# Performance work log

Measured on AMD Instinct MI355X. Metric: run time of the kernel, lower is better.

The kernel has to match this reference:

```python
import jax, jax.numpy as jnp
import numpy as np

N_NODES = 100000
N_EDGES = 1600000
NODE_F = 64
EDGE_F = 16
OUT_F = 64


def setup_inputs() -> dict:
    key = jax.random.key(0)
    k1, k2, k3, k4, k5 = jax.random.split(key, 5)
    feat = jax.random.normal(k1, (N_NODES, NODE_F), dtype=jnp.float32)
    edge_feats = jax.random.normal(k2, (N_EDGES, EDGE_F), dtype=jnp.float32)
    src = jax.random.randint(k3, (N_EDGES,), 0, N_NODES, dtype=jnp.int64)
    dst = jax.random.randint(k4, (N_EDGES,), 0, N_NODES, dtype=jnp.int64)
    # xavier-normal-ish weight, zero bias (matches reset_parameters)
    fan_in, fan_out = NODE_F + EDGE_F, OUT_F
    std = (2.0 / (fan_in + fan_out)) ** 0.5
    weight = jax.random.normal(k5, (fan_in, fan_out), dtype=jnp.float32) * std
    bias = jnp.zeros((OUT_F,), dtype=jnp.float32)
    return {"feat": feat, "edge_feats": edge_feats, "src": src, "dst": dst,
            "weight": weight, "bias": bias}


def reference(feat, edge_feats, src, dst, weight, bias):
    N = feat.shape[0]
    # in-degree based symmetric-ish norm: pow(clamp(in_deg,1), -0.5)
    deg = jax.ops.segment_sum(jnp.ones(dst.shape, dtype=feat.dtype), dst,
                              num_segments=N)
    norm = jnp.clip(deg, 1.0) ** -0.5  # [N]
    norm = norm[:, None]
    # sum over incoming edges of concat([edge_feats, h_src]).
    # sum of concat == concat of sums, so aggregate each part separately
    # (avoids materializing the per-edge concat).
    sum_e = jax.ops.segment_sum(edge_feats, dst, num_segments=N)  # [N, E_F]
    sum_h = jax.ops.segment_sum(feat[src], dst, num_segments=N)   # [N, NODE_F]
    sum_f = jnp.concatenate([sum_e, sum_h], axis=-1)              # [N, E_F+NODE_F]
    out = (sum_f * norm) @ weight
    out = out * norm + bias
    return jax.nn.selu(out)
```

## Files before the change

kernel.cpp:

```cpp
#include <hip/hip_runtime.h>
#include <math.h>

#define N_NODES 100000
#define N_EDGES 1600000
#define OUT_F   64
#define NCHUNK  98

#define EQ4      (N_EDGES / 4)
#define CNT_BLK  ((EQ4 + 255) / 256)
#define GEMM_BLK 512
#define K_E      18

typedef __attribute__((ext_vector_type(8))) short bf16x8;
typedef __attribute__((ext_vector_type(4))) float f32x4;

__device__ __forceinline__ unsigned short f2bf_rne(float f) {
    unsigned u = __float_as_uint(f);
    return (unsigned short)((u + 0x7fffu + ((u >> 16) & 1u)) >> 16);
}
__device__ __forceinline__ float bf2f(unsigned short h) {
    return __uint_as_float((unsigned)h << 16);
}

__global__ __launch_bounds__(256) void count_gemm(
    const int* __restrict__ dst, unsigned* __restrict__ bsum,
    const float* __restrict__ feat, const float* __restrict__ weight,
    unsigned short* __restrict__ G)
{
    __shared__ unsigned lbin[NCHUNK];
    int tid = threadIdx.x;

    if (blockIdx.x < CNT_BLK) {
        if (tid < NCHUNK) lbin[tid] = 0u;
        __syncthreads();
        int q = blockIdx.x * 256 + tid;
        if (q < EQ4) {
            int4 d = ((const int4*)dst)[q];
            atomicAdd(&lbin[d.x >> 10], 1u);
            atomicAdd(&lbin[d.y >> 10], 1u);
            atomicAdd(&lbin[d.z >> 10], 1u);
            atomicAdd(&lbin[d.w >> 10], 1u);
        }
        __syncthreads();
        if (tid < NCHUNK) {
            unsigned v = lbin[tid];
            if (v) atomicAdd(&bsum[tid], v);
        }
        return;
    }

    int gb = (int)blockIdx.x - CNT_BLK;
    int wv = tid >> 6, ln = tid & 63;
    int li = ln & 15, lk = ln >> 4;

    bf16x8 Whi[4][2], Wlo[4][2];
    #pragma unroll
    for (int it = 0; it < 4; ++it)
        #pragma unroll
        for (int kb = 0; kb < 2; ++kb)
            #pragma unroll
            for (int j = 0; j < 8; ++j) {
                float w = weight[(16 + kb * 32 + lk * 8 + j) * 64 + it * 16 + li];
                unsigned short h = f2bf_rne(w);
                Whi[it][kb][j] = (short)h;
                Wlo[it][kb][j] = (short)f2bf_rne(w - bf2f(h));
            }

    const int tiles = N_NODES / 16;
    for (int tile = gb * 4 + wv; tile < tiles; tile += GEMM_BLK * 4) {
        int n = tile * 16 + li;
        const float* fr = feat + (size_t)n * 64 + lk * 8;

        bf16x8 Bhi[2], Blo[2];
        #pragma unroll
        for (int kb = 0; kb < 2; ++kb) {
            float4 v0 = *(const float4*)(fr + kb * 32);
            float4 v1 = *(const float4*)(fr + kb * 32 + 4);
            float vv[8] = {v0.x, v0.y, v0.z, v0.w, v1.x, v1.y, v1.z, v1.w};
            #pragma unroll
            for (int j = 0; j < 8; ++j) {
                unsigned short h = f2bf_rne(vv[j]);
                Bhi[kb][j] = (short)h;
                Blo[kb][j] = (short)f2bf_rne(vv[j] - bf2f(h));
            }
        }

        f32x4 acc[4] = {{0.f,0.f,0.f,0.f},{0.f,0.f,0.f,0.f},
                        {0.f,0.f,0.f,0.f},{0.f,0.f,0.f,0.f}};
        #pragma unroll
        for (int kb = 0; kb < 2; ++kb)
            #pragma unroll
            for (int it = 0; it < 4; ++it) {
                acc[it] = __builtin_amdgcn_mfma_f32_16x16x32_bf16(Whi[it][kb], Bhi[kb], acc[it], 0, 0, 0);
                acc[it] = __builtin_amdgcn_mfma_f32_16x16x32_bf16(Wlo[it][kb], Bhi[kb], acc[it], 0, 0, 0);
                acc[it] = __builtin_amdgcn_mfma_f32_16x16x32_bf16(Whi[it][kb], Blo[kb], acc[it], 0, 0, 0);
            }

        #pragma unroll
        for (int it = 0; it < 4; ++it) {
            ushort4 o;
            o.x = f2bf_rne(acc[it][0]);
            o.y = f2bf_rne(acc[it][1]);
            o.z = f2bf_rne(acc[it][2]);
            o.w = f2bf_rne(acc[it][3]);
            *(ushort4*)(G + (size_t)n * 64 + it * 16 + lk * 4) = o;
        }
    }
}

__global__ __launch_bounds__(256) void bucket_scatter(
    const int* __restrict__ src, const int* __restrict__ dst,
    const unsigned* __restrict__ bsum, unsigned* __restrict__ cursor,
    unsigned long long* __restrict__ csr_pack)
{
    __shared__ unsigned ob[128], bb[128];
    __shared__ unsigned cnt[NCHUNK];
    __shared__ unsigned gb[NCHUNK];
    int tid = threadIdx.x;

    if (tid < 128) {
        unsigned v = (tid < NCHUNK) ? bsum[tid] : 0u;
        ob[tid] = v; bb[tid] = v;
    }
    if (tid < NCHUNK) cnt[tid] = 0u;
    __syncthreads();
    #pragma unroll
    for (int o = 1; o < 128; o <<= 1) {
        unsigned u = (tid < 128 && tid >= o) ? bb[tid - o] : 0u;
        __syncthreads();
        if (tid < 128) bb[tid] += u;
        __syncthreads();
    }

    int q = blockIdx.x * 256 + tid;
    bool act = q < EQ4;
    int4 d = {0,0,0,0}, s = {0,0,0,0};
    unsigned r0 = 0, r1 = 0, r2 = 0, r3 = 0;
    if (act) {
        d = ((const int4*)dst)[q];
        s = ((const int4*)src)[q];
        r0 = atomicAdd(&cnt[d.x >> 10], 1u);
        r1 = atomicAdd(&cnt[d.y >> 10], 1u);
        r2 = atomicAdd(&cnt[d.z >> 10], 1u);
        r3 = atomicAdd(&cnt[d.w >> 10], 1u);
    }
    __syncthreads();
    if (tid < NCHUNK) {
        unsigned c = cnt[tid];
        unsigned res = c ? atomicAdd(&cursor[tid], c) : 0u;
        gb[tid] = res + bb[tid] - ob[tid];
    }
    __syncthreads();
    if (act) {
        unsigned e = (unsigned)q * 4u;
        csr_pack[gb[d.x >> 10] + r0] =
            (unsigned long long)((unsigned)s.x | (((unsigned)d.x & 1023u) << 20))
            | ((unsigned long long)(e + 0u) << 32);
        csr_pack[gb[d.y >> 10] + r1] =
            (unsigned long long)((unsigned)s.y | (((unsigned)d.y & 1023u) << 20))
            | ((unsigned long long)(e + 1u) << 32);
        csr_pack[gb[d.z >> 10] + r2] =
            (unsigned long long)((unsigned)s.z | (((unsigned)d.z & 1023u) << 20))
            | ((unsigned long long)(e + 2u) << 32);
        csr_pack[gb[d.w >> 10] + r3] =
            (unsigned long long)((unsigned)s.w | (((unsigned)d.w & 1023u) << 20))
            | ((unsigned long long)(e + 3u) << 32);
    }
}

__global__ __launch_bounds__(1024) void chunk_build(
    const unsigned* __restrict__ bsum, unsigned* __restrict__ off,
    unsigned long long* __restrict__ csr_pack)
{
    __shared__ unsigned ob[128], bb[128];
    __shared__ unsigned cnt[1024];
    __shared__ unsigned ws[16];
    int t = threadIdx.x, c = blockIdx.x;

    if (t < 128) {
        unsigned v = (t < NCHUNK) ? bsum[t] : 0u;
        ob[t] = v; bb[t] = v;
    }
    cnt[t] = 0u;
    __syncthreads();
    #pragma unroll
    for (int o = 1; o < 128; o <<= 1) {
        unsigned u = (t < 128 && t >= o) ? bb[t - o] : 0u;
        __syncthreads();
        if (t < 128) bb[t] += u;
        __syncthreads();
    }
    unsigned base = bb[c] - ob[c];
    unsigned ne   = ob[c];
    __syncthreads();

    unsigned long long ev[K_E];
    unsigned rk[K_E];
    #pragma unroll
    for (int k = 0; k < K_E; ++k) {
        unsigned i = (unsigned)t + (unsigned)k * 1024u;
        if (i < ne) {
            ev[k] = csr_pack[base + i];
            rk[k] = atomicAdd(&cnt[(unsigned)(ev[k] >> 20) & 1023u], 1u);
        }
    }
    __syncthreads();

    unsigned v = cnt[t];
    unsigned x = v;
    #pragma unroll
    for (int o = 1; o < 64; o <<= 1) {
        unsigned u = __shfl_up(x, o);
        if ((t & 63) >= o) x += u;
    }
    if ((t & 63) == 63) ws[t >> 6] = x;
    __syncthreads();
    if (t < 16) {
        unsigned y = ws[t];
        #pragma unroll
        for (int o = 1; o < 16; o <<= 1) {
            unsigned u = __shfl_up(y, o);
            if (t >= o) y += u;
        }
        ws[t] = y;
    }
    __syncthreads();
    unsigned excl = ((t >> 6) ? ws[(t >> 6) - 1] : 0u) + x - v;

    int gnode = c * 1024 + t;
    if (gnode < N_NODES) off[gnode] = base + excl;
    if (c == NCHUNK - 1 && t == 0) off[N_NODES] = N_EDGES;

    __syncthreads();
    cnt[t] = base + excl;
    __syncthreads();

    #pragma unroll
    for (int k = 0; k < K_E; ++k) {
        unsigned i = (unsigned)t + (unsigned)k * 1024u;
        if (i < ne) {
            unsigned dl = (unsigned)(ev[k] >> 20) & 1023u;
            csr_pack[cnt[dl] + rk[k]] = ev[k] & 0xFFFFFFFF000FFFFFull;
        }
    }
}

__global__ __launch_bounds__(256) void gather_out(
    const unsigned short* __restrict__ G,
    const float* __restrict__ edge_feats,
    const unsigned long long* __restrict__ csr_pack,
    const unsigned* __restrict__ off,
    const float* __restrict__ weight,
    const float* __restrict__ bias,
    float* __restrict__ out)
{
    int tid = threadIdx.x;
    int wv = tid >> 6, ln = tid & 63;

    float We[16];
    #pragma unroll
    for (int k = 0; k < 16; ++k) We[k] = weight[k * 64 + ln];
    float b = bias[ln];

    const float SC = 1.0507009873554805f;
    const float AL = 1.6732632423543772f;

    int n = blockIdx.x * 4 + wv;
    if (n >= N_NODES) return;

    unsigned start = off[n], end = off[n + 1];
    float norm2 = __builtin_amdgcn_rcpf(fmaxf((float)(end - start), 1.0f));

    const int gq = ln >> 4;
    const int eq = ln >> 2;

    float gh4[4] = {0.f, 0.f, 0.f, 0.f};
    float ae4[4] = {0.f, 0.f, 0.f, 0.f};

    const ushort4* __restrict__ Gv = (const ushort4*)G;

    for (unsigned base = start; base < end; base += 64u) {
        unsigned m = min(64u, end - base);
        unsigned lo = 0u, hi = 0u;
        if ((unsigned)ln < m) {
            unsigned long long pk = csr_pack[base + (unsigned)ln];
            lo = (unsigned)pk;
            hi = (unsigned)(pk >> 32);
        }

        for (unsigned i = 0; i < m; i += 8u) {
            unsigned i0 = i + (unsigned)gq, i1 = i0 + 4u;
            unsigned s0 = __shfl(lo, (int)min(i0, m - 1u));
            unsigned s1 = __shfl(lo, (int)min(i1, m - 1u));
            ushort4 q0 = {0,0,0,0}, q1 = {0,0,0,0};
            if (i0 < m) q0 = Gv[(size_t)s0 * 16u + (unsigned)(ln & 15)];
            if (i1 < m) q1 = Gv[(size_t)s1 * 16u + (unsigned)(ln & 15)];
            gh4[0] += __uint_as_float((unsigned)q0.x << 16) + __uint_as_float((unsigned)q1.x << 16);
            gh4[1] += __uint_as_float((unsigned)q0.y << 16) + __uint_as_float((unsigned)q1.y << 16);
            gh4[2] += __uint_as_float((unsigned)q0.z << 16) + __uint_as_float((unsigned)q1.z << 16);
            gh4[3] += __uint_as_float((unsigned)q0.w << 16) + __uint_as_float((unsigned)q1.w << 16);
        }

        for (unsigned i = 0; i < m; i += 16u) {
            unsigned ie = i + (unsigned)eq;
            unsigned e0 = __shfl(hi, (int)min(ie, m - 1u));
            if (ie < m) {
                float4 v = *(const float4*)(edge_feats + (size_t)e0 * 16u + (unsigned)(ln & 3) * 4u);
                ae4[0] += v.x; ae4[1] += v.y; ae4[2] += v.z; ae4[3] += v.w;
            }
        }
    }

    #pragma unroll
    for (int c = 0; c < 4; ++c) {
        gh4[c] += __shfl_xor(gh4[c], 16);
        gh4[c] += __shfl_xor(gh4[c], 32);
        ae4[c] += __shfl_xor(ae4[c], 4);
        ae4[c] += __shfl_xor(ae4[c], 8);
        ae4[c] += __shfl_xor(ae4[c], 16);
        ae4[c] += __shfl_xor(ae4[c], 32);
    }
    int srcl = ln >> 2;
    float r0 = __shfl(gh4[0], srcl);
    float r1 = __shfl(gh4[1], srcl);
    float r2 = __shfl(gh4[2], srcl);
    float r3 = __shfl(gh4[3], srcl);
    int c = ln & 3;
    float gh = (c & 2) ? ((c & 1) ? r3 : r2) : ((c & 1) ? r1 : r0);

    float acc = gh;
    #pragma unroll
    for (int k = 0; k < 16; ++k)
        acc = fmaf(__shfl(ae4[k & 3], k >> 2), We[k], acc);

    float o = acc * norm2 + b;
    out[(size_t)n * 64u + ln] = (o > 0.f) ? SC * o : SC * AL * (__expf(o) - 1.0f);
}

extern "C" void kernel_launch(void* const* d_in, const int* in_sizes, int n_in,
                              void* d_out, int out_size, void* d_ws, size_t ws_size,
                              hipStream_t stream) {
    const float* feat       = (const float*)d_in[0];
    const float* edge_feats = (const float*)d_in[1];
    const int*   src        = (const int*)d_in[2];
    const int*   dst        = (const int*)d_in[3];
    const float* weight     = (const float*)d_in[4];
    const float* bias       = (const float*)d_in[5];
    float* out = (float*)d_out;

    unsigned long long* csr_pack = (unsigned long long*)d_ws;
    unsigned short* G = (unsigned short*)(csr_pack + N_EDGES);
    unsigned* off    = (unsigned*)(G + (size_t)N_NODES * 64);
    unsigned* bsum   = off + N_NODES + 1;
    unsigned* cursor = bsum + NCHUNK;

    hipMemsetAsync(bsum, 0, 2 * NCHUNK * sizeof(unsigned), stream);
    count_gemm<<<dim3(CNT_BLK + GEMM_BLK), dim3(256), 0, stream>>>(
        dst, bsum, feat, weight, G);
    bucket_scatter<<<dim3(CNT_BLK), dim3(256), 0, stream>>>(
        src, dst, bsum, cursor, csr_pack);
    chunk_build<<<dim3(NCHUNK), dim3(1024), 0, stream>>>(bsum, off, csr_pack);
    gather_out<<<dim3((N_NODES + 3) / 4), dim3(256), 0, stream>>>(
        G, edge_feats, csr_pack, off, weight, bias, out);
}
```

Baseline: 370.2 us.

## Replace global atomic bucket cursors with deterministic per-block count scan

Count blocks now write per-block bucket histograms instead of atomically accumulating into a global sum. Two new small kernels column-scan those histograms and scan the chunk totals, so the scatter kernel gets exact per-block offsets without global atomics on a cursor. This also drops the memset and the redundant 128-wide prefix scans repeated in every scatter and chunk_build block. It costs two extra kernel launches and extra histogram traffic (CNT_BLK×98 words written and read twice).

```diff
diff --git a/kernel.cpp b/kernel.cpp
--- a/kernel.cpp
+++ b/kernel.cpp
@@ -23,7 +23,7 @@
 }
 
 __global__ __launch_bounds__(256) void count_gemm(
-    const int* __restrict__ dst, unsigned* __restrict__ bsum,
+    const int* __restrict__ dst, unsigned* __restrict__ pcnt,
     const float* __restrict__ feat, const float* __restrict__ weight,
     unsigned short* __restrict__ G)
 {
@@ -42,10 +42,8 @@
             atomicAdd(&lbin[d.w >> 10], 1u);
         }
         __syncthreads();
-        if (tid < NCHUNK) {
-            unsigned v = lbin[tid];
-            if (v) atomicAdd(&bsum[tid], v);
-        }
+        if (tid < NCHUNK)
+            pcnt[(size_t)blockIdx.x * NCHUNK + tid] = lbin[tid];
         return;
     }
 
@@ -108,29 +106,69 @@
     }
 }
 
-__global__ __launch_bounds__(256) void bucket_scatter(
+__global__ __launch_bounds__(1024) void colscan(
+    const unsigned* __restrict__ pcnt, unsigned* __restrict__ pbase,
+    unsigned* __restrict__ ctot)
+{
+    __shared__ unsigned ws[16];
+    int c = blockIdx.x, t = threadIdx.x;
+    unsigned j0 = 2u * (unsigned)t, j1 = j0 + 1u;
+    unsigned v0 = (j0 < CNT_BLK) ? pcnt[(size_t)j0 * NCHUNK + c] : 0u;
+    unsigned v1 = (j1 < CNT_BLK) ? pcnt[(size_t)j1 * NCHUNK + c] : 0u;
+    unsigned s = v0 + v1;
+    unsigned x = s;
+    #pragma unroll
+    for (int o = 1; o < 64; o <<= 1) {
+        unsigned u = __shfl_up(x, o);
+        if ((t & 63) >= o) x += u;
+    }
+    if ((t & 63) == 63) ws[t >> 6] = x;
+    __syncthreads();
+    if (t < 16) {
+        unsigned y = ws[t];
+        #pragma unroll
+        for (int o = 1; o < 16; o <<= 1) {
+            unsigned u = __shfl_up(y, o);
+            if (t >= o) y += u;
+        }
+        ws[t] = y;
+    }
+    __syncthreads();
+    unsigned excl = ((t >> 6) ? ws[(t >> 6) - 1] : 0u) + x - s;
+    if (j0 < CNT_BLK) pbase[(size_t)j0 * NCHUNK + c] = excl;
+    if (j1 < CNT_BLK) pbase[(size_t)j1 * NCHUNK + c] = excl + v0;
+    if (t == 1023) ctot[c] = excl + s;
+}
+
+__global__ __launch_bounds__(128) void scan98(
+    const unsigned* __restrict__ ctot, unsigned* __restrict__ cbase)
+{
+    __shared__ unsigned w0;
+    int t = threadIdx.x;
+    unsigned v = (t < NCHUNK) ? ctot[t] : 0u;
+    unsigned x = v;
+    #pragma unroll
+    for (int o = 1; o < 64; o <<= 1) {
+        unsigned u = __shfl_up(x, o);
+        if ((t & 63) >= o) x += u;
+    }
+    if (t == 63) w0 = x;
+    __syncthreads();
+    unsigned base = (t >= 64) ? w0 : 0u;
+    if (t < NCHUNK) cbase[t] = base + x - v;
+}
+
+__global__ __launch_bounds__(256) void scatter(
     const int* __restrict__ src, const int* __restrict__ dst,
-    const unsigned* __restrict__ bsum, unsigned* __restrict__ cursor,
+    const unsigned* __restrict__ pbase, const unsigned* __restrict__ cbase,
     unsigned long long* __restrict__ csr_pack)
 {
-    __shared__ unsigned ob[128], bb[128];
     __shared__ unsigned cnt[NCHUNK];
     __shared__ unsigned gb[NCHUNK];
     int tid = threadIdx.x;
 
-    if (tid < 128) {
-        unsigned v = (tid < NCHUNK) ? bsum[tid] : 0u;
-        ob[tid] = v; bb[tid] = v;
-    }
     if (tid < NCHUNK) cnt[tid] = 0u;
     __syncthreads();
-    #pragma unroll
-    for (int o = 1; o < 128; o <<= 1) {
-        unsigned u = (tid < 128 && tid >= o) ? bb[tid - o] : 0u;
-        __syncthreads();
-        if (tid < 128) bb[tid] += u;
-        __syncthreads();
-    }
 
     int q = blockIdx.x * 256 + tid;
     bool act = q < EQ4;
@@ -144,12 +182,8 @@
         r2 = atomicAdd(&cnt[d.z >> 10], 1u);
         r3 = atomicAdd(&cnt[d.w >> 10], 1u);
     }
-    __syncthreads();
-    if (tid < NCHUNK) {
-        unsigned c = cnt[tid];
-        unsigned res = c ? atomicAdd(&cursor[tid], c) : 0u;
-        gb[tid] = res + bb[tid] - ob[tid];
-    }
+    if (tid < NCHUNK)
+        gb[tid] = cbase[tid] + pbase[(size_t)blockIdx.x * NCHUNK + tid];
     __syncthreads();
     if (act) {
         unsigned e = (unsigned)q * 4u;
@@ -169,29 +203,16 @@
 }
 
 __global__ __launch_bounds__(1024) void chunk_build(
-    const unsigned* __restrict__ bsum, unsigned* __restrict__ off,
-    unsigned long long* __restrict__ csr_pack)
-{
-    __shared__ unsigned ob[128], bb[128];
+    const unsigned* __restrict__ ctot, const unsigned* __restrict__ cbase,
+    unsigned* __restrict__ off, unsigned long long* __restrict__ csr_pack)
+{
     __shared__ unsigned cnt[1024];
     __shared__ unsigned ws[16];
     int t = threadIdx.x, c = blockIdx.x;
 
-    if (t < 128) {
-        unsigned v = (t < NCHUNK) ? bsum[t] : 0u;
-        ob[t] = v; bb[t] = v;
-    }
+    unsigned base = cbase[c];
+    unsigned ne   = ctot[c];
     cnt[t] = 0u;
-    __syncthreads();
-    #pragma unroll
-    for (int o = 1; o < 128; o <<= 1) {
-        unsigned u = (t < 128 && t >= o) ? bb[t - o] : 0u;
-        __syncthreads();
-        if (t < 128) bb[t] += u;
-        __syncthreads();
-    }
-    unsigned base = bb[c] - ob[c];
-    unsigned ne   = ob[c];
     __syncthreads();
 
     unsigned long long ev[K_E];
@@ -350,16 +371,20 @@
 
     unsigned long long* csr_pack = (unsigned long long*)d_ws;
     unsigned short* G = (unsigned short*)(csr_pack + N_EDGES);
-    unsigned* off    = (unsigned*)(G + (size_t)N_NODES * 64);
-    unsigned* bsum   = off + N_NODES + 1;
-    unsigned* cursor = bsum + NCHUNK;
-
-    hipMemsetAsync(bsum, 0, 2 * NCHUNK * sizeof(unsigned), stream);
+    unsigned* off   = (unsigned*)(G + (size_t)N_NODES * 64);
+    unsigned* pcnt  = off + N_NODES + 1;
+    unsigned* pbase = pcnt + (size_t)CNT_BLK * NCHUNK;
+    unsigned* ctot  = pbase + (size_t)CNT_BLK * NCHUNK;
+    unsigned* cbase = ctot + NCHUNK;
+
     count_gemm<<<dim3(CNT_BLK + GEMM_BLK), dim3(256), 0, stream>>>(
-        dst, bsum, feat, weight, G);
-    bucket_scatter<<<dim3(CNT_BLK), dim3(256), 0, stream>>>(
-        src, dst, bsum, cursor, csr_pack);
-    chunk_build<<<dim3(NCHUNK), dim3(1024), 0, stream>>>(bsum, off, csr_pack);
+        dst, pcnt, feat, weight, G);
+    colscan<<<dim3(NCHUNK), dim3(1024), 0, stream>>>(pcnt, pbase, ctot);
+    scan98<<<dim3(1), dim3(128), 0, stream>>>(ctot, cbase);
+    scatter<<<dim3(CNT_BLK), dim3(256), 0, stream>>>(
+        src, dst, pbase, cbase, csr_pack);
+    chunk_build<<<dim3(NCHUNK), dim3(1024), 0, stream>>>(
+        ctot, cbase, off, csr_pack);
     gather_out<<<dim3((N_NODES + 3) / 4), dim3(256), 0, stream>>>(
         G, edge_feats, csr_pack, off, weight, bias, out);
 }
```

Measured after the change: 297.6 us. 19.6% less time.
